# Kernel tuning notes

Measured on AMD Instinct MI355X. Metric: run time of the kernel, lower is better.

## Reference

```python
import jax, jax.numpy as jnp
import numpy as np
from jax import lax

B, L = 4, 1024
D_MODEL, D_INNER, D_STATE, D_CONV, DT_RANK, N_LAYERS = 256, 512, 16, 4, 16, 4
BN_EPS = 1e-5


def setup_inputs() -> dict:
    key = jax.random.key(0)
    ks = jax.random.split(key, 16)
    nrm = lambda k, s, sc: jax.random.normal(k, s, jnp.float32) * sc
    inp = {
        "x": nrm(ks[0], (B, L), 1.0),
        "y": nrm(ks[1], (B, L), 1.0),  # accepted but unused by forward
        # embedding: Conv1d(1 -> D_MODEL, k=3, same, no bias) + BatchNorm1d (inference stats) + SiLU
        "emb_w": nrm(ks[2], (D_MODEL, 1, 3), 1.0 / np.sqrt(3.0)),
        "bn_gamma": 1.0 + nrm(ks[3], (D_MODEL,), 0.1),
        "bn_beta": nrm(ks[4], (D_MODEL,), 0.1),
        "bn_mean": nrm(ks[5], (D_MODEL,), 0.1),
        "bn_var": jax.random.uniform(ks[6], (D_MODEL,), jnp.float32, 0.5, 1.5),
        # stacked Mamba layer params (leading dim = layer)
        "in_proj_w": nrm(ks[7], (N_LAYERS, 2 * D_INNER, D_MODEL), 1.0 / np.sqrt(D_MODEL)),
        "conv_w": nrm(ks[8], (N_LAYERS, D_INNER, 1, D_CONV), 1.0 / np.sqrt(D_CONV)),
        "conv_b": nrm(ks[9], (N_LAYERS, D_INNER), 0.02),
        "x_proj_w": nrm(ks[10], (N_LAYERS, DT_RANK + 2 * D_STATE, D_INNER), 1.0 / np.sqrt(D_INNER)),
        "dt_proj_w": nrm(ks[11], (N_LAYERS, D_INNER, DT_RANK), 1.0 / np.sqrt(DT_RANK)),
        # inverse-softplus of dt in [1e-3, 0.1] (mamba init)
        "dt_proj_b": jnp.log(jnp.expm1(jax.random.uniform(ks[12], (N_LAYERS, D_INNER), jnp.float32, 1e-3, 0.1))),
        # S4D-real init: A = -[1..N]
        "A_log": jnp.log(jnp.tile(jnp.arange(1, D_STATE + 1, dtype=jnp.float32)[None, None, :], (N_LAYERS, D_INNER, 1))),
        "D_skip": jnp.ones((N_LAYERS, D_INNER), jnp.float32),
        "out_proj_w": nrm(ks[13], (N_LAYERS, D_MODEL, D_INNER), 1.0 / np.sqrt(D_INNER)),
    }
    return inp


def selective_scan(u, dt, A, Bc, Cc, D_skip):
    # u, dt: (B,L,Di); A: (Di,N); Bc, Cc: (B,L,N)
    dA = jnp.exp(dt[..., None] * A)                              # (B,L,Di,N)
    dBu = dt[..., None] * Bc[:, :, None, :] * u[..., None]       # (B,L,Di,N)

    def step(h, xs):
        dA_t, dBu_t, C_t = xs
        h = dA_t * h + dBu_t                                      # (B,Di,N)
        y_t = jnp.einsum('bdn,bn->bd', h, C_t)
        return h, y_t

    h0 = jnp.zeros((u.shape[0], u.shape[2], A.shape[1]), u.dtype)
    _, ys = lax.scan(step, h0, (dA.swapaxes(0, 1), dBu.swapaxes(0, 1), Cc.swapaxes(0, 1)))
    return ys.swapaxes(0, 1) + u * D_skip                         # (B,L,Di)


def mamba_block(h, in_w, cw, cb, xp_w, dtp_w, dtp_b, A_log, D_skip, out_w):
    xz = jnp.einsum('bld,ed->ble', h, in_w)                       # (B,L,2Di)
    xi, z = jnp.split(xz, 2, axis=-1)
    # causal depthwise conv1d over time
    xc = lax.conv_general_dilated(xi.swapaxes(1, 2), cw, (1,), [(D_CONV - 1, 0)],
                                  dimension_numbers=('NCH', 'OIH', 'NCH'),
                                  feature_group_count=D_INNER) + cb[None, :, None]
    xc = jax.nn.silu(xc).swapaxes(1, 2)                           # (B,L,Di)
    xdbl = jnp.einsum('bld,ed->ble', xc, xp_w)                    # (B,L,dt_rank+2N)
    dt, Bc, Cc = jnp.split(xdbl, [DT_RANK, DT_RANK + D_STATE], axis=-1)
    dt = jax.nn.softplus(jnp.einsum('blr,dr->bld', dt, dtp_w) + dtp_b)
    A = -jnp.exp(A_log)                                           # (Di,N)
    y = selective_scan(xc, dt, A, Bc, Cc, D_skip)
    y = y * jax.nn.silu(z)
    return jnp.einsum('bld,od->blo', y, out_w)                    # (B,L,D_MODEL)


def reference(x, y, emb_w, bn_gamma, bn_beta, bn_mean, bn_var, in_proj_w, conv_w,
              conv_b, x_proj_w, dt_proj_w, dt_proj_b, A_log, D_skip, out_proj_w):
    h = x[:, None, :]                                             # (B,1,L)
    h = lax.conv_general_dilated(h, emb_w, (1,), 'SAME', dimension_numbers=('NCH', 'OIH', 'NCH'))
    inv = lax.rsqrt(bn_var + BN_EPS)
    h = (h - bn_mean[None, :, None]) * (inv * bn_gamma)[None, :, None] + bn_beta[None, :, None]
    h = jax.nn.silu(h).swapaxes(1, 2)                             # (B,L,D_MODEL)
    for i in range(N_LAYERS):
        h = mamba_block(h, in_proj_w[i], conv_w[i], conv_b[i], x_proj_w[i],
                        dt_proj_w[i], dt_proj_b[i], A_log[i], D_skip[i], out_proj_w[i])
    return h.sum(axis=-1)                                         # (B,L)
```

## Files before the change

kernel.cpp:

```cpp
#include <hip/hip_runtime.h>
#include <math.h>

#define BATCH 4
#define SEQL 1024
#define DMODEL 256
#define DINNER 512
#define DSTATE 16
#define DTRANK 16
#define NLAYERS 4
#define MTOT (BATCH * SEQL)

#define IDX(t) ((((t) & 63) * 17) + ((t) >> 6))

#define LOG2E 1.44269504088896340736f

typedef float v2f __attribute__((ext_vector_type(2)));

static __device__ __forceinline__ v2f pkfma(v2f a, v2f b, v2f c) {
    return __builtin_elementwise_fma(a, b, c);
}
static __device__ __forceinline__ float exp2fast(float x) {
    return __builtin_amdgcn_exp2f(x);
}
static __device__ __forceinline__ float siluf(float x) {
    return x / (1.0f + __expf(-x));
}
static __device__ __forceinline__ float softplusf(float x) {
    return (x > 0.0f) ? (x + __logf(1.0f + __expf(-x))) : __logf(1.0f + __expf(x));
}

__global__ void k_embed(const float* __restrict__ x, const float* __restrict__ emb_w,
                        const float* __restrict__ gamma, const float* __restrict__ beta,
                        const float* __restrict__ mean, const float* __restrict__ var,
                        float* __restrict__ h) {
    const int m = blockIdx.x;
    const int d = threadIdx.x;
    const int b = m >> 10;
    const int l = m & 1023;
    const float xm1 = (l > 0)    ? x[b * SEQL + l - 1] : 0.0f;
    const float x0  =              x[b * SEQL + l];
    const float xp1 = (l < 1023) ? x[b * SEQL + l + 1] : 0.0f;
    float c = xm1 * emb_w[d * 3 + 0] + x0 * emb_w[d * 3 + 1] + xp1 * emb_w[d * 3 + 2];
    const float inv = 1.0f / sqrtf(var[d] + 1e-5f);
    c = (c - mean[d]) * (inv * gamma[d]) + beta[d];
    h[(size_t)m * DMODEL + d] = siluf(c);
}

template <int BM, int BN, int BK, int TM, int TN, bool AKM, int KTOT, int KSPLIT>
__global__ __launch_bounds__((BM / TM) * (BN / TN))
void sgemm2(const float* __restrict__ A, int lda,
            const float* __restrict__ Bw, int ldb,
            float* __restrict__ C, int ldc, int mstride) {
    constexpr int TX = BN / TN;
    constexpr int TY = BM / TM;
    constexpr int NT = TX * TY;
    static_assert(NT == 256, "expect 256 threads");
    constexpr int KS = KTOT / KSPLIT;
    static_assert(KS % BK == 0, "");
    constexpr int NSTEPS = KS / BK;
    constexpr int A4 = BM * BK / 4;
    constexpr int B4 = BN * BK / 4;
    constexpr int APT = (A4 + NT - 1) / NT;
    constexpr int BPT = (B4 + NT - 1) / NT;
    constexpr bool AG = (A4 % NT) != 0;
    constexpr bool BG = (B4 % NT) != 0;

    const int tid = threadIdx.x;
    const int tx = tid % TX;
    const int ty = tid / TX;
    const int m0 = blockIdx.y * BM;
    const int n0 = blockIdx.x * BN;
    const int kt0 = blockIdx.z * KS;

    __shared__ float As[BK][BM + 4];
    __shared__ float Bs[BK][BN + 4];

    float acc[TM][TN] = {};
    float4 ra[APT], rb[BPT];

    auto loadA = [&](int kt) {
#pragma unroll
        for (int u = 0; u < APT; ++u) {
            const int v = tid + u * NT;
            if (!AG || v < A4) {
                if (AKM) {
                    const int kk = v / (BM / 4);
                    const int i4 = v % (BM / 4);
                    ra[u] = *reinterpret_cast<const float4*>(
                        &A[(size_t)(kt + kk) * lda + m0 + i4 * 4]);
                } else {
                    const int i = v / (BK / 4);
                    const int jv = v % (BK / 4);
                    ra[u] = *reinterpret_cast<const float4*>(
                        &A[(size_t)(m0 + i) * lda + kt + jv * 4]);
                }
            }
        }
    };
    auto loadB = [&](int kt) {
#pragma unroll
        for (int u = 0; u < BPT; ++u) {
            const int v = tid + u * NT;
            if (!BG || v < B4) {
                const int i = v / (BK / 4);
                const int jv = v % (BK / 4);
                rb[u] = *reinterpret_cast<const float4*>(
                    &Bw[(size_t)(n0 + i) * ldb + kt + jv * 4]);
            }
        }
    };
    auto storeAB = [&]() {
#pragma unroll
        for (int u = 0; u < APT; ++u) {
            const int v = tid + u * NT;
            if (!AG || v < A4) {
                if (AKM) {
                    const int kk = v / (BM / 4);
                    const int i4 = v % (BM / 4);
                    *reinterpret_cast<float4*>(&As[kk][i4 * 4]) = ra[u];
                } else {
                    const int i = v / (BK / 4);
                    const int jv = v % (BK / 4);
                    As[jv * 4 + 0][i] = ra[u].x;
                    As[jv * 4 + 1][i] = ra[u].y;
                    As[jv * 4 + 2][i] = ra[u].z;
                    As[jv * 4 + 3][i] = ra[u].w;
                }
            }
        }
#pragma unroll
        for (int u = 0; u < BPT; ++u) {
            const int v = tid + u * NT;
            if (!BG || v < B4) {
                const int i = v / (BK / 4);
                const int jv = v % (BK / 4);
                Bs[jv * 4 + 0][i] = rb[u].x;
                Bs[jv * 4 + 1][i] = rb[u].y;
                Bs[jv * 4 + 2][i] = rb[u].z;
                Bs[jv * 4 + 3][i] = rb[u].w;
            }
        }
    };

    loadA(kt0);
    loadB(kt0);

    for (int s = 0; s < NSTEPS; ++s) {
        storeAB();
        __syncthreads();
        if (s + 1 < NSTEPS) {
            loadA(kt0 + (s + 1) * BK);
            loadB(kt0 + (s + 1) * BK);
        }
#pragma unroll
        for (int k = 0; k < BK; ++k) {
            float a[TM], b[TN];
#pragma unroll
            for (int i = 0; i < TM; ++i) a[i] = As[k][ty * TM + i];
#pragma unroll
            for (int j = 0; j < TN; ++j) b[j] = Bs[k][tx * TN + j];
#pragma unroll
            for (int i = 0; i < TM; ++i)
#pragma unroll
                for (int j = 0; j < TN; ++j) acc[i][j] = fmaf(a[i], b[j], acc[i][j]);
        }
        __syncthreads();
    }

    float* Cz = C + (size_t)blockIdx.z * mstride;
#pragma unroll
    for (int i = 0; i < TM; ++i) {
        const int m = m0 + ty * TM + i;
#pragma unroll
        for (int j = 0; j < TN; ++j) {
            const int n = n0 + tx * TN + j;
            Cz[(size_t)m * ldc + n] = acc[i][j];
        }
    }
}

template <int BM, int BN, int BK, int TM, int TN, bool AKM, int KTOT, int KSPLIT>
__global__ __launch_bounds__((BM / TM) * (BN / TN))
void sgemm3(const float* __restrict__ A, int lda,
            const float* __restrict__ Bw, int ldb,
            float* __restrict__ C, int ldc, int mstride) {
    constexpr int TX = BN / TN;
    constexpr int TY = BM / TM;
    constexpr int NT = TX * TY;
    static_assert(NT == 256, "expect 256 threads");
    static_assert(TN % 2 == 0, "packed needs even TN");
    constexpr int TN2 = TN / 2;
    constexpr int KS = KTOT / KSPLIT;
    static_assert(KS % BK == 0, "");
    constexpr int NSTEPS = KS / BK;
    constexpr int A4 = BM * BK / 4;
    constexpr int B4 = BN * BK / 4;
    constexpr int APT = (A4 + NT - 1) / NT;
    constexpr int BPT = (B4 + NT - 1) / NT;
    constexpr bool AG = (A4 % NT) != 0;
    constexpr bool BG = (B4 % NT) != 0;

    const int tid = threadIdx.x;
    const int tx = tid % TX;
    const int ty = tid / TX;
    const int m0 = blockIdx.y * BM;
    const int n0 = blockIdx.x * BN;
    const int kt0 = blockIdx.z * KS;

    __shared__ float As[BK][BM + 4];
    __shared__ float Bs[BK][BN + 4];

    v2f acc[TM][TN2] = {};
    float4 ra[APT], rb[BPT];

    auto loadA = [&](int kt) {
#pragma unroll
        for (int u = 0; u < APT; ++u) {
            const int v = tid + u * NT;
            if (!AG || v < A4) {
                if (AKM) {
                    const int kk = v / (BM / 4);
                    const int i4 = v % (BM / 4);
                    ra[u] = *reinterpret_cast<const float4*>(
                        &A[(size_t)(kt + kk) * lda + m0 + i4 * 4]);
                } else {
                    const int i = v / (BK / 4);
                    const int jv = v % (BK / 4);
                    ra[u] = *reinterpret_cast<const float4*>(
                        &A[(size_t)(m0 + i) * lda + kt + jv * 4]);
                }
            }
        }
    };
    auto loadB = [&](int kt) {
#pragma unroll
        for (int u = 0; u < BPT; ++u) {
            const int v = tid + u * NT;
            if (!BG || v < B4) {
                const int i = v / (BK / 4);
                const int jv = v % (BK / 4);
                rb[u] = *reinterpret_cast<const float4*>(
                    &Bw[(size_t)(n0 + i) * ldb + kt + jv * 4]);
            }
        }
    };
    auto storeAB = [&]() {
#pragma unroll
        for (int u = 0; u < APT; ++u) {
            const int v = tid + u * NT;
            if (!AG || v < A4) {
                if (AKM) {
                    const int kk = v / (BM / 4);
                    const int i4 = v % (BM / 4);
                    *reinterpret_cast<float4*>(&As[kk][i4 * 4]) = ra[u];
                } else {
                    const int i = v / (BK / 4);
                    const int jv = v % (BK / 4);
                    As[jv * 4 + 0][i] = ra[u].x;
                    As[jv * 4 + 1][i] = ra[u].y;
                    As[jv * 4 + 2][i] = ra[u].z;
                    As[jv * 4 + 3][i] = ra[u].w;
                }
            }
        }
#pragma unroll
        for (int u = 0; u < BPT; ++u) {
            const int v = tid + u * NT;
            if (!BG || v < B4) {
                const int i = v / (BK / 4);
                const int jv = v % (BK / 4);
                Bs[jv * 4 + 0][i] = rb[u].x;
                Bs[jv * 4 + 1][i] = rb[u].y;
                Bs[jv * 4 + 2][i] = rb[u].z;
                Bs[jv * 4 + 3][i] = rb[u].w;
            }
        }
    };

    loadA(kt0);
    loadB(kt0);

    for (int s = 0; s < NSTEPS; ++s) {
        storeAB();
        __syncthreads();
        if (s + 1 < NSTEPS) {
            loadA(kt0 + (s + 1) * BK);
            loadB(kt0 + (s + 1) * BK);
        }
#pragma unroll
        for (int k = 0; k < BK; ++k) {
            float a[TM];
            v2f b2[TN2];
#pragma unroll
            for (int i = 0; i < TM; ++i) a[i] = As[k][ty * TM + i];
#pragma unroll
            for (int j = 0; j < TN2; ++j)
                b2[j] = *reinterpret_cast<const v2f*>(&Bs[k][tx * TN + 2 * j]);
#pragma unroll
            for (int i = 0; i < TM; ++i) {
                v2f av;
                av.x = a[i]; av.y = a[i];
#pragma unroll
                for (int j = 0; j < TN2; ++j) acc[i][j] = pkfma(av, b2[j], acc[i][j]);
            }
        }
        __syncthreads();
    }

    float* Cz = C + (size_t)blockIdx.z * mstride;
#pragma unroll
    for (int i = 0; i < TM; ++i) {
        const int m = m0 + ty * TM + i;
#pragma unroll
        for (int j = 0; j < TN2; ++j) {
            *reinterpret_cast<v2f*>(&Cz[(size_t)m * ldc + n0 + tx * TN + 2 * j]) =
                acc[i][j];
        }
    }
}

template <int KS>
__global__ __launch_bounds__(512) void k_kred(const float* __restrict__ part,
                                              float* __restrict__ out, int n4) {
    const int i = blockIdx.x * 512 + threadIdx.x;
    if (i >= n4) return;
    const float4* p = reinterpret_cast<const float4*>(part);
    float4 s = p[i];
#pragma unroll
    for (int z = 1; z < KS; ++z) {
        const float4 t = p[i + (size_t)z * n4];
        s.x += t.x; s.y += t.y; s.z += t.z; s.w += t.w;
    }
    reinterpret_cast<float4*>(out)[i] = s;
}

__global__ __launch_bounds__(256) void k_convT4(const float* __restrict__ xzT,
                                                const float* __restrict__ cw,
                                                const float* __restrict__ cb,
                                                float* __restrict__ xcT) {
    const int d = blockIdx.x;
    const int b = blockIdx.y;
    const float w0 = cw[d * 4 + 0], w1 = cw[d * 4 + 1];
    const float w2 = cw[d * 4 + 2], w3 = cw[d * 4 + 3];
    const float bias = cb[d];
    const float* row = xzT + (size_t)d * MTOT + b * SEQL;
    float* orow = xcT + (size_t)d * MTOT + b * SEQL;
    const int t4 = threadIdx.x * 4;
    const float4 xv = *reinterpret_cast<const float4*>(&row[t4]);
    float4 xm = make_float4(0.f, 0.f, 0.f, 0.f);
    if (t4 >= 4) xm = *reinterpret_cast<const float4*>(&row[t4 - 4]);
    float4 o;
    o.x = fmaf(xv.x, w3, fmaf(xm.w, w2, fmaf(xm.z, w1, fmaf(xm.y, w0, bias))));
    o.y = fmaf(xv.y, w3, fmaf(xv.x, w2, fmaf(xm.w, w1, fmaf(xm.z, w0, bias))));
    o.z = fmaf(xv.z, w3, fmaf(xv.y, w2, fmaf(xv.x, w1, fmaf(xm.w, w0, bias))));
    o.w = fmaf(xv.w, w3, fmaf(xv.z, w2, fmaf(xv.y, w1, fmaf(xv.x, w0, bias))));
    o.x = siluf(o.x); o.y = siluf(o.y); o.z = siluf(o.z); o.w = siluf(o.w);
    *reinterpret_cast<float4*>(&orow[t4]) = o;
}

#define CCH 64
#define CT 16

__global__ __launch_bounds__(256) void k_scan10(
    const float* __restrict__ xcT, const float* __restrict__ xdbl,
    const float* __restrict__ xzT, const float* __restrict__ dtw,
    const float* __restrict__ dtb, const float* __restrict__ A_log,
    const float* __restrict__ D_skip, float* __restrict__ yT) {
    const int d = blockIdx.x;
    const int b = blockIdx.y;
    const int tid = threadIdx.x;
    const int c = tid >> 2;
    const int nq = tid & 3;

    __shared__ float dt_s[1088];
    __shared__ float u_s[1088];
    __shared__ __align__(16) float PSp[CCH][20];
    __shared__ __align__(16) float PSs[CCH][20];

    const int mbase = b * SEQL;

    const float4 w0 = *reinterpret_cast<const float4*>(&dtw[d * 16 + 0]);
    const float4 w1 = *reinterpret_cast<const float4*>(&dtw[d * 16 + 4]);
    const float4 w2 = *reinterpret_cast<const float4*>(&dtw[d * 16 + 8]);
    const float4 w3 = *reinterpret_cast<const float4*>(&dtw[d * 16 + 12]);
    const float bias = dtb[d];

#pragma unroll
    for (int ph = 0; ph < 4; ++ph) {
        const int t = ph * 256 + tid;
        const float* xr = &xdbl[(size_t)(mbase + t) * 48];
        const float4 a0 = *reinterpret_cast<const float4*>(&xr[0]);
        const float4 a1 = *reinterpret_cast<const float4*>(&xr[4]);
        const float4 a2v = *reinterpret_cast<const float4*>(&xr[8]);
        const float4 a3 = *reinterpret_cast<const float4*>(&xr[12]);
        v2f s2; s2.x = bias; s2.y = 0.0f;
        v2f p, q;
        p.x = a0.x;  p.y = a0.y;  q.x = w0.x;  q.y = w0.y;  s2 = pkfma(p, q, s2);
        p.x = a0.z;  p.y = a0.w;  q.x = w0.z;  q.y = w0.w;  s2 = pkfma(p, q, s2);
        p.x = a1.x;  p.y = a1.y;  q.x = w1.x;  q.y = w1.y;  s2 = pkfma(p, q, s2);
        p.x = a1.z;  p.y = a1.w;  q.x = w1.z;  q.y = w1.w;  s2 = pkfma(p, q, s2);
        p.x = a2v.x; p.y = a2v.y; q.x = w2.x;  q.y = w2.y;  s2 = pkfma(p, q, s2);
        p.x = a2v.z; p.y = a2v.w; q.x = w2.z;  q.y = w2.w;  s2 = pkfma(p, q, s2);
        p.x = a3.x;  p.y = a3.y;  q.x = w3.x;  q.y = w3.y;  s2 = pkfma(p, q, s2);
        p.x = a3.z;  p.y = a3.w;  q.x = w3.z;  q.y = w3.w;  s2 = pkfma(p, q, s2);
        const float dt = softplusf(s2.x + s2.y);
        const float uv = xcT[(size_t)d * MTOT + mbase + t];
        dt_s[IDX(t)] = dt;
        u_s[IDX(t)]  = dt * uv;
    }
    __syncthreads();

    const float4 al = *reinterpret_cast<const float4*>(&A_log[d * DSTATE + nq * 4]);
    v2f a01, a23;
    a01.x = -__expf(al.x) * LOG2E;
    a01.y = -__expf(al.y) * LOG2E;
    a23.x = -__expf(al.z) * LOG2E;
    a23.y = -__expf(al.w) * LOG2E;

    const int t0 = c * CT;
    const int loc_base = (c & 3) * 272 + (c >> 2);

    const float* Bp = &xdbl[(size_t)(mbase + t0) * 48 + DTRANK + nq * 4];
    const float* Cp = Bp + DSTATE;

    float dtsum = 0.0f;
    v2f S01, S23;
    S01.x = S01.y = S23.x = S23.y = 0.0f;
#pragma unroll
    for (int j = 0; j < CT; ++j) {
        const float4 B4 = *reinterpret_cast<const float4*>(&Bp[j * 48]);
        const int loc = j * 17 + loc_base;
        const float dtv = dt_s[loc];
        const float du = u_s[loc];
        dtsum += dtv;
        v2f dd; dd.x = dtv; dd.y = dtv;
        v2f duv; duv.x = du; duv.y = du;
        const v2f t01 = dd * a01;
        const v2f t23 = dd * a23;
        v2f e01, e23;
        e01.x = exp2fast(t01.x); e01.y = exp2fast(t01.y);
        e23.x = exp2fast(t23.x); e23.y = exp2fast(t23.y);
        v2f B01, B23;
        B01.x = B4.x; B01.y = B4.y; B23.x = B4.z; B23.y = B4.w;
        S01 = pkfma(e01, S01, B01 * duv);
        S23 = pkfma(e23, S23, B23 * duv);
    }
    {
        float4 Pq, Sq;
        Pq.x = exp2fast(a01.x * dtsum);
        Pq.y = exp2fast(a01.y * dtsum);
        Pq.z = exp2fast(a23.x * dtsum);
        Pq.w = exp2fast(a23.y * dtsum);
        Sq.x = S01.x; Sq.y = S01.y; Sq.z = S23.x; Sq.w = S23.y;
        *reinterpret_cast<float4*>(&PSp[c][nq * 4]) = Pq;
        *reinterpret_cast<float4*>(&PSs[c][nq * 4]) = Sq;
    }
    __syncthreads();

    v2f h01, h23;
    h01.x = h01.y = h23.x = h23.y = 0.0f;
    for (int j = 0; j < c; ++j) {
        const float4 qp = *reinterpret_cast<const float4*>(&PSp[j][nq * 4]);
        const float4 qs = *reinterpret_cast<const float4*>(&PSs[j][nq * 4]);
        v2f pp, ss;
        pp.x = qp.x; pp.y = qp.y; ss.x = qs.x; ss.y = qs.y;
        h01 = pkfma(pp, h01, ss);
        pp.x = qp.z; pp.y = qp.w; ss.x = qs.z; ss.y = qs.w;
        h23 = pkfma(pp, h23, ss);
    }

#pragma unroll
    for (int j = 0; j < CT; ++j) {
        const float4 B4 = *reinterpret_cast<const float4*>(&Bp[j * 48]);
        const float4 C4 = *reinterpret_cast<const float4*>(&Cp[j * 48]);
        const int loc = j * 17 + loc_base;
        const float dtv = dt_s[loc];
        const float du = u_s[loc];
        v2f dd; dd.x = dtv; dd.y = dtv;
        v2f duv; duv.x = du; duv.y = du;
        const v2f t01 = dd * a01;
        const v2f t23 = dd * a23;
        v2f e01, e23;
        e01.x = exp2fast(t01.x); e01.y = exp2fast(t01.y);
        e23.x = exp2fast(t23.x); e23.y = exp2fast(t23.y);
        v2f B01, B23;
        B01.x = B4.x; B01.y = B4.y; B23.x = B4.z; B23.y = B4.w;
        h01 = pkfma(e01, h01, B01 * duv);
        h23 = pkfma(e23, h23, B23 * duv);
        v2f C01, C23;
        C01.x = C4.x; C01.y = C4.y; C23.x = C4.z; C23.y = C4.w;
        v2f tt = h01 * C01;
        tt = pkfma(h23, C23, tt);
        float p = tt.x + tt.y;
        p += __shfl_xor(p, 1);
        p += __shfl_xor(p, 2);
        if (nq == 0) dt_s[loc] = p;
    }
    __syncthreads();

    const float Dsk = D_skip[d];
#pragma unroll
    for (int ph = 0; ph < 4; ++ph) {
        const int t = ph * 256 + tid;
        const float uv = xcT[(size_t)d * MTOT + mbase + t];
        const float zv = xzT[(size_t)(DINNER + d) * MTOT + mbase + t];
        yT[(size_t)d * MTOT + mbase + t] = (dt_s[IDX(t)] + uv * Dsk) * siluf(zv);
    }
}

__global__ void k_wsum(const float* __restrict__ w, float* __restrict__ wsum) {
    const int d = threadIdx.x;
    float s = 0.0f;
    for (int o = 0; o < DMODEL; ++o) s += w[(size_t)o * DINNER + d];
    wsum[d] = s;
}

__global__ __launch_bounds__(256) void k_finalT(const float* __restrict__ yT,
                                                const float* __restrict__ wsum,
                                                float* __restrict__ out) {
    const int tid = threadIdx.x;
    const int dg = tid >> 5;
    const int ml = tid & 31;
    const int m = blockIdx.x * 32 + ml;
    float acc = 0.0f;
    const int dbase = dg * 64;
#pragma unroll 8
    for (int dd = 0; dd < 64; ++dd)
        acc = fmaf(yT[(size_t)(dbase + dd) * MTOT + m], wsum[dbase + dd], acc);
    __shared__ float red[8][33];
    red[dg][ml] = acc;
    __syncthreads();
    if (dg == 0) {
        float s = 0.0f;
#pragma unroll
        for (int g = 0; g < 8; ++g) s += red[g][ml];
        out[m] = s;
    }
}

extern "C" void kernel_launch(void* const* d_in, const int* in_sizes, int n_in,
                              void* d_out, int out_size, void* d_ws, size_t ws_size,
                              hipStream_t stream) {
    const float* x        = (const float*)d_in[0];
    const float* emb_w    = (const float*)d_in[2];
    const float* bn_gamma = (const float*)d_in[3];
    const float* bn_beta  = (const float*)d_in[4];
    const float* bn_mean  = (const float*)d_in[5];
    const float* bn_var   = (const float*)d_in[6];
    const float* in_proj_w  = (const float*)d_in[7];
    const float* conv_w     = (const float*)d_in[8];
    const float* conv_b     = (const float*)d_in[9];
    const float* x_proj_w   = (const float*)d_in[10];
    const float* dt_proj_w  = (const float*)d_in[11];
    const float* dt_proj_b  = (const float*)d_in[12];
    const float* A_log      = (const float*)d_in[13];
    const float* D_skip     = (const float*)d_in[14];
    const float* out_proj_w = (const float*)d_in[15];
    float* out = (float*)d_out;
    float* ws = (float*)d_ws;

    float* h    = ws;
    float* xzT  = h + (size_t)MTOT * DMODEL;
    float* xcT  = xzT + (size_t)1024 * MTOT;
    float* xdbl = xcT + (size_t)DINNER * MTOT;
    float* yT   = xdbl + (size_t)MTOT * 48;
    float* wsum = yT + (size_t)DINNER * MTOT;
    float* partX = yT;
    float* partO = xzT;

    k_embed<<<MTOT, DMODEL, 0, stream>>>(x, emb_w, bn_gamma, bn_beta, bn_mean, bn_var, h);

    for (int i = 0; i < NLAYERS; ++i) {
        const float* in_w  = in_proj_w + (size_t)i * 2 * DINNER * DMODEL;
        const float* cw    = conv_w + (size_t)i * DINNER * 4;
        const float* cb    = conv_b + (size_t)i * DINNER;
        const float* xp_w  = x_proj_w + (size_t)i * 48 * DINNER;
        const float* dtp_w = dt_proj_w + (size_t)i * DINNER * DTRANK;
        const float* dtp_b = dt_proj_b + (size_t)i * DINNER;
        const float* Al    = A_log + (size_t)i * DINNER * DSTATE;
        const float* Dsk   = D_skip + (size_t)i * DINNER;
        const float* o_w   = out_proj_w + (size_t)i * DMODEL * DINNER;

        sgemm3<64, 128, 16, 4, 8, false, DMODEL, 1>
            <<<dim3(MTOT / 128, 1024 / 64, 1), 256, 0, stream>>>(
                in_w, DMODEL, h, DMODEL, xzT, MTOT, 0);

        k_convT4<<<dim3(DINNER, BATCH), 256, 0, stream>>>(xzT, cw, cb, xcT);

        sgemm2<64, 48, 16, 4, 3, true, DINNER, 8>
            <<<dim3(1, MTOT / 64, 8), 256, 0, stream>>>(
                xcT, MTOT, xp_w, DINNER, partX, 48, MTOT * 48);
        k_kred<8><<<(MTOT * 48 / 4 + 511) / 512, 512, 0, stream>>>(
            partX, xdbl, MTOT * 48 / 4);

        k_scan10<<<dim3(DINNER, BATCH), 256, 0, stream>>>(
            xcT, xdbl, xzT, dtp_w, dtp_b, Al, Dsk, yT);

        if (i < NLAYERS - 1) {
            sgemm3<64, 64, 16, 4, 4, true, DINNER, 2>
                <<<dim3(DMODEL / 64, MTOT / 64, 2), 256, 0, stream>>>(
                    yT, MTOT, o_w, DINNER, partO, DMODEL, MTOT * DMODEL);
            k_kred<2><<<(MTOT * DMODEL / 4 + 511) / 512, 512, 0, stream>>>(
                partO, h, MTOT * DMODEL / 4);
        } else {
            k_wsum<<<1, DINNER, 0, stream>>>(o_w, wsum);
            k_finalT<<<MTOT / 32, 256, 0, stream>>>(yT, wsum, out);
        }
    }
}
```

Before: 438.0 us.

## Fuse causal conv into x_proj and scan, fold split-K reduce into in_proj

Removes the standalone depthwise conv kernel and the xcT buffer: the conv+SiLU is recomputed inline when loading the A tile of the x_proj GEMM and again in the scan kernel from xzT. The out_proj split-K partial reduction kernel is dropped by summing the two partial buffers while loading the B operand of the next layer's in_proj GEMM, with partO given its own workspace region. This saves several launches and a full read/write pass of intermediate activations, at the cost of redundant conv arithmetic and extra scalar loads in the scan.

```diff
diff --git a/kernel.cpp b/kernel.cpp
--- a/kernel.cpp
+++ b/kernel.cpp
@@ -46,15 +46,18 @@
     h[(size_t)m * DMODEL + d] = siluf(c);
 }
 
-template <int BM, int BN, int BK, int TM, int TN, bool AKM, int KTOT, int KSPLIT>
+template <int BM, int BN, int BK, int TM, int TN, bool AKM, int KTOT, int KSPLIT,
+          bool BSUM>
 __global__ __launch_bounds__((BM / TM) * (BN / TN))
-void sgemm2(const float* __restrict__ A, int lda,
-            const float* __restrict__ Bw, int ldb,
+void sgemm3(const float* __restrict__ A, int lda,
+            const float* __restrict__ Bw, const float* __restrict__ Bw2, int ldb,
             float* __restrict__ C, int ldc, int mstride) {
     constexpr int TX = BN / TN;
     constexpr int TY = BM / TM;
     constexpr int NT = TX * TY;
     static_assert(NT == 256, "expect 256 threads");
+    static_assert(TN % 2 == 0, "packed needs even TN");
+    constexpr int TN2 = TN / 2;
     constexpr int KS = KTOT / KSPLIT;
     static_assert(KS % BK == 0, "");
     constexpr int NSTEPS = KS / BK;
@@ -75,7 +78,7 @@
     __shared__ float As[BK][BM + 4];
     __shared__ float Bs[BK][BN + 4];
 
-    float acc[TM][TN] = {};
+    v2f acc[TM][TN2] = {};
     float4 ra[APT], rb[BPT];
 
     auto loadA = [&](int kt) {
@@ -104,8 +107,13 @@
             if (!BG || v < B4) {
                 const int i = v / (BK / 4);
                 const int jv = v % (BK / 4);
-                rb[u] = *reinterpret_cast<const float4*>(
-                    &Bw[(size_t)(n0 + i) * ldb + kt + jv * 4]);
+                const size_t off = (size_t)(n0 + i) * ldb + kt + jv * 4;
+                rb[u] = *reinterpret_cast<const float4*>(&Bw[off]);
+                if (BSUM) {
+                    const float4 t2 = *reinterpret_cast<const float4*>(&Bw2[off]);
+                    rb[u].x += t2.x; rb[u].y += t2.y;
+                    rb[u].z += t2.z; rb[u].w += t2.w;
+                }
             }
         }
     };
@@ -154,15 +162,20 @@
         }
 #pragma unroll
         for (int k = 0; k < BK; ++k) {
-            float a[TM], b[TN];
+            float a[TM];
+            v2f b2[TN2];
 #pragma unroll
             for (int i = 0; i < TM; ++i) a[i] = As[k][ty * TM + i];
 #pragma unroll
-            for (int j = 0; j < TN; ++j) b[j] = Bs[k][tx * TN + j];
-#pragma unroll
-            for (int i = 0; i < TM; ++i)
-#pragma unroll
-                for (int j = 0; j < TN; ++j) acc[i][j] = fmaf(a[i], b[j], acc[i][j]);
+            for (int j = 0; j < TN2; ++j)
+                b2[j] = *reinterpret_cast<const v2f*>(&Bs[k][tx * TN + 2 * j]);
+#pragma unroll
+            for (int i = 0; i < TM; ++i) {
+                v2f av;
+                av.x = a[i]; av.y = a[i];
+#pragma unroll
+                for (int j = 0; j < TN2; ++j) acc[i][j] = pkfma(av, b2[j], acc[i][j]);
+            }
         }
         __syncthreads();
     }
@@ -172,108 +185,74 @@
     for (int i = 0; i < TM; ++i) {
         const int m = m0 + ty * TM + i;
 #pragma unroll
-        for (int j = 0; j < TN; ++j) {
-            const int n = n0 + tx * TN + j;
-            Cz[(size_t)m * ldc + n] = acc[i][j];
-        }
-    }
-}
-
-template <int BM, int BN, int BK, int TM, int TN, bool AKM, int KTOT, int KSPLIT>
-__global__ __launch_bounds__((BM / TM) * (BN / TN))
-void sgemm3(const float* __restrict__ A, int lda,
-            const float* __restrict__ Bw, int ldb,
-            float* __restrict__ C, int ldc, int mstride) {
+        for (int j = 0; j < TN2; ++j) {
+            *reinterpret_cast<v2f*>(&Cz[(size_t)m * ldc + n0 + tx * TN + 2 * j]) =
+                acc[i][j];
+        }
+    }
+}
+
+__global__ __launch_bounds__(256)
+void sgemm_xp(const float* __restrict__ xzT, const float* __restrict__ cw,
+              const float* __restrict__ cb, const float* __restrict__ Bw,
+              float* __restrict__ C, int mstride) {
+    constexpr int BM = 64, BN = 48, BK = 16, TM = 4, TN = 3;
     constexpr int TX = BN / TN;
-    constexpr int TY = BM / TM;
-    constexpr int NT = TX * TY;
-    static_assert(NT == 256, "expect 256 threads");
-    static_assert(TN % 2 == 0, "packed needs even TN");
-    constexpr int TN2 = TN / 2;
-    constexpr int KS = KTOT / KSPLIT;
-    static_assert(KS % BK == 0, "");
+    constexpr int KS = DINNER / 8;
     constexpr int NSTEPS = KS / BK;
-    constexpr int A4 = BM * BK / 4;
     constexpr int B4 = BN * BK / 4;
-    constexpr int APT = (A4 + NT - 1) / NT;
-    constexpr int BPT = (B4 + NT - 1) / NT;
-    constexpr bool AG = (A4 % NT) != 0;
-    constexpr bool BG = (B4 % NT) != 0;
 
     const int tid = threadIdx.x;
     const int tx = tid % TX;
     const int ty = tid / TX;
     const int m0 = blockIdx.y * BM;
-    const int n0 = blockIdx.x * BN;
     const int kt0 = blockIdx.z * KS;
 
     __shared__ float As[BK][BM + 4];
     __shared__ float Bs[BK][BN + 4];
 
-    v2f acc[TM][TN2] = {};
-    float4 ra[APT], rb[BPT];
+    float acc[TM][TN] = {};
+    float4 ra;
+    float4 rb;
 
     auto loadA = [&](int kt) {
-#pragma unroll
-        for (int u = 0; u < APT; ++u) {
-            const int v = tid + u * NT;
-            if (!AG || v < A4) {
-                if (AKM) {
-                    const int kk = v / (BM / 4);
-                    const int i4 = v % (BM / 4);
-                    ra[u] = *reinterpret_cast<const float4*>(
-                        &A[(size_t)(kt + kk) * lda + m0 + i4 * 4]);
-                } else {
-                    const int i = v / (BK / 4);
-                    const int jv = v % (BK / 4);
-                    ra[u] = *reinterpret_cast<const float4*>(
-                        &A[(size_t)(m0 + i) * lda + kt + jv * 4]);
-                }
-            }
-        }
+        const int kk = tid >> 4;
+        const int i4 = tid & 15;
+        const int r = kt + kk;
+        const float* row = xzT + (size_t)r * MTOT;
+        const int t4 = m0 + i4 * 4;
+        const float4 xv = *reinterpret_cast<const float4*>(&row[t4]);
+        float4 xm = make_float4(0.f, 0.f, 0.f, 0.f);
+        if ((t4 & 1023) >= 4) xm = *reinterpret_cast<const float4*>(&row[t4 - 4]);
+        const float4 w = *reinterpret_cast<const float4*>(&cw[r * 4]);
+        const float bias = cb[r];
+        float4 o;
+        o.x = fmaf(xv.x, w.w, fmaf(xm.w, w.z, fmaf(xm.z, w.y, fmaf(xm.y, w.x, bias))));
+        o.y = fmaf(xv.y, w.w, fmaf(xv.x, w.z, fmaf(xm.w, w.y, fmaf(xm.z, w.x, bias))));
+        o.z = fmaf(xv.z, w.w, fmaf(xv.y, w.z, fmaf(xv.x, w.y, fmaf(xm.w, w.x, bias))));
+        o.w = fmaf(xv.w, w.w, fmaf(xv.z, w.z, fmaf(xv.y, w.y, fmaf(xv.x, w.x, bias))));
+        o.x = siluf(o.x); o.y = siluf(o.y); o.z = siluf(o.z); o.w = siluf(o.w);
+        ra = o;
     };
     auto loadB = [&](int kt) {
-#pragma unroll
-        for (int u = 0; u < BPT; ++u) {
-            const int v = tid + u * NT;
-            if (!BG || v < B4) {
-                const int i = v / (BK / 4);
-                const int jv = v % (BK / 4);
-                rb[u] = *reinterpret_cast<const float4*>(
-                    &Bw[(size_t)(n0 + i) * ldb + kt + jv * 4]);
-            }
+        if (tid < B4) {
+            const int i = tid / (BK / 4);
+            const int jv = tid % (BK / 4);
+            rb = *reinterpret_cast<const float4*>(
+                &Bw[(size_t)i * DINNER + kt + jv * 4]);
         }
     };
     auto storeAB = [&]() {
-#pragma unroll
-        for (int u = 0; u < APT; ++u) {
-            const int v = tid + u * NT;
-            if (!AG || v < A4) {
-                if (AKM) {
-                    const int kk = v / (BM / 4);
-                    const int i4 = v % (BM / 4);
-                    *reinterpret_cast<float4*>(&As[kk][i4 * 4]) = ra[u];
-                } else {
-                    const int i = v / (BK / 4);
-                    const int jv = v % (BK / 4);
-                    As[jv * 4 + 0][i] = ra[u].x;
-                    As[jv * 4 + 1][i] = ra[u].y;
-                    As[jv * 4 + 2][i] = ra[u].z;
-                    As[jv * 4 + 3][i] = ra[u].w;
-                }
-            }
-        }
-#pragma unroll
-        for (int u = 0; u < BPT; ++u) {
-            const int v = tid + u * NT;
-            if (!BG || v < B4) {
-                const int i = v / (BK / 4);
-                const int jv = v % (BK / 4);
-                Bs[jv * 4 + 0][i] = rb[u].x;
-                Bs[jv * 4 + 1][i] = rb[u].y;
-                Bs[jv * 4 + 2][i] = rb[u].z;
-                Bs[jv * 4 + 3][i] = rb[u].w;
-            }
+        const int kk = tid >> 4;
+        const int i4 = tid & 15;
+        *reinterpret_cast<float4*>(&As[kk][i4 * 4]) = ra;
+        if (tid < B4) {
+            const int i = tid / (BK / 4);
+            const int jv = tid % (BK / 4);
+            Bs[jv * 4 + 0][i] = rb.x;
+            Bs[jv * 4 + 1][i] = rb.y;
+            Bs[jv * 4 + 2][i] = rb.z;
+            Bs[jv * 4 + 3][i] = rb.w;
         }
     };
 
@@ -289,20 +268,15 @@
         }
 #pragma unroll
         for (int k = 0; k < BK; ++k) {
-            float a[TM];
-            v2f b2[TN2];
+            float a[TM], b[TN];
 #pragma unroll
             for (int i = 0; i < TM; ++i) a[i] = As[k][ty * TM + i];
 #pragma unroll
-            for (int j = 0; j < TN2; ++j)
-                b2[j] = *reinterpret_cast<const v2f*>(&Bs[k][tx * TN + 2 * j]);
-#pragma unroll
-            for (int i = 0; i < TM; ++i) {
-                v2f av;
-                av.x = a[i]; av.y = a[i];
-#pragma unroll
-                for (int j = 0; j < TN2; ++j) acc[i][j] = pkfma(av, b2[j], acc[i][j]);
-            }
+            for (int j = 0; j < TN; ++j) b[j] = Bs[k][tx * TN + j];
+#pragma unroll
+            for (int i = 0; i < TM; ++i)
+#pragma unroll
+                for (int j = 0; j < TN; ++j) acc[i][j] = fmaf(a[i], b[j], acc[i][j]);
         }
         __syncthreads();
     }
@@ -312,10 +286,8 @@
     for (int i = 0; i < TM; ++i) {
         const int m = m0 + ty * TM + i;
 #pragma unroll
-        for (int j = 0; j < TN2; ++j) {
-            *reinterpret_cast<v2f*>(&Cz[(size_t)m * ldc + n0 + tx * TN + 2 * j]) =
-                acc[i][j];
-        }
+        for (int j = 0; j < TN; ++j)
+            Cz[(size_t)m * 48 + tx * TN + j] = acc[i][j];
     }
 }
 
@@ -334,38 +306,15 @@
     reinterpret_cast<float4*>(out)[i] = s;
 }
 
-__global__ __launch_bounds__(256) void k_convT4(const float* __restrict__ xzT,
-                                                const float* __restrict__ cw,
-                                                const float* __restrict__ cb,
-                                                float* __restrict__ xcT) {
-    const int d = blockIdx.x;
-    const int b = blockIdx.y;
-    const float w0 = cw[d * 4 + 0], w1 = cw[d * 4 + 1];
-    const float w2 = cw[d * 4 + 2], w3 = cw[d * 4 + 3];
-    const float bias = cb[d];
-    const float* row = xzT + (size_t)d * MTOT + b * SEQL;
-    float* orow = xcT + (size_t)d * MTOT + b * SEQL;
-    const int t4 = threadIdx.x * 4;
-    const float4 xv = *reinterpret_cast<const float4*>(&row[t4]);
-    float4 xm = make_float4(0.f, 0.f, 0.f, 0.f);
-    if (t4 >= 4) xm = *reinterpret_cast<const float4*>(&row[t4 - 4]);
-    float4 o;
-    o.x = fmaf(xv.x, w3, fmaf(xm.w, w2, fmaf(xm.z, w1, fmaf(xm.y, w0, bias))));
-    o.y = fmaf(xv.y, w3, fmaf(xv.x, w2, fmaf(xm.w, w1, fmaf(xm.z, w0, bias))));
-    o.z = fmaf(xv.z, w3, fmaf(xv.y, w2, fmaf(xv.x, w1, fmaf(xm.w, w0, bias))));
-    o.w = fmaf(xv.w, w3, fmaf(xv.z, w2, fmaf(xv.y, w1, fmaf(xv.x, w0, bias))));
-    o.x = siluf(o.x); o.y = siluf(o.y); o.z = siluf(o.z); o.w = siluf(o.w);
-    *reinterpret_cast<float4*>(&orow[t4]) = o;
-}
-
 #define CCH 64
 #define CT 16
 
-__global__ __launch_bounds__(256) void k_scan10(
-    const float* __restrict__ xcT, const float* __restrict__ xdbl,
-    const float* __restrict__ xzT, const float* __restrict__ dtw,
-    const float* __restrict__ dtb, const float* __restrict__ A_log,
-    const float* __restrict__ D_skip, float* __restrict__ yT) {
+__global__ __launch_bounds__(256) void k_scan11(
+    const float* __restrict__ xdbl, const float* __restrict__ xzT,
+    const float* __restrict__ dtw, const float* __restrict__ dtb,
+    const float* __restrict__ cw, const float* __restrict__ cb,
+    const float* __restrict__ A_log, const float* __restrict__ D_skip,
+    float* __restrict__ yT) {
     const int d = blockIdx.x;
     const int b = blockIdx.y;
     const int tid = threadIdx.x;
@@ -378,12 +327,15 @@
     __shared__ __align__(16) float PSs[CCH][20];
 
     const int mbase = b * SEQL;
+    const float* xrow = xzT + (size_t)d * MTOT + mbase;
 
     const float4 w0 = *reinterpret_cast<const float4*>(&dtw[d * 16 + 0]);
     const float4 w1 = *reinterpret_cast<const float4*>(&dtw[d * 16 + 4]);
     const float4 w2 = *reinterpret_cast<const float4*>(&dtw[d * 16 + 8]);
     const float4 w3 = *reinterpret_cast<const float4*>(&dtw[d * 16 + 12]);
     const float bias = dtb[d];
+    const float4 cwv = *reinterpret_cast<const float4*>(&cw[d * 4]);
+    const float cbias = cb[d];
 
 #pragma unroll
     for (int ph = 0; ph < 4; ++ph) {
@@ -404,7 +356,13 @@
         p.x = a3.x;  p.y = a3.y;  q.x = w3.x;  q.y = w3.y;  s2 = pkfma(p, q, s2);
         p.x = a3.z;  p.y = a3.w;  q.x = w3.z;  q.y = w3.w;  s2 = pkfma(p, q, s2);
         const float dt = softplusf(s2.x + s2.y);
-        const float uv = xcT[(size_t)d * MTOT + mbase + t];
+        const float xt  = xrow[t];
+        const float xt1 = (t >= 1) ? xrow[t - 1] : 0.0f;
+        const float xt2 = (t >= 2) ? xrow[t - 2] : 0.0f;
+        const float xt3 = (t >= 3) ? xrow[t - 3] : 0.0f;
+        float cv = fmaf(xt, cwv.w, fmaf(xt1, cwv.z,
+                   fmaf(xt2, cwv.y, fmaf(xt3, cwv.x, cbias))));
+        const float uv = siluf(cv);
         dt_s[IDX(t)] = dt;
         u_s[IDX(t)]  = dt * uv;
     }
@@ -502,7 +460,13 @@
 #pragma unroll
     for (int ph = 0; ph < 4; ++ph) {
         const int t = ph * 256 + tid;
-        const float uv = xcT[(size_t)d * MTOT + mbase + t];
+        const float xt  = xrow[t];
+        const float xt1 = (t >= 1) ? xrow[t - 1] : 0.0f;
+        const float xt2 = (t >= 2) ? xrow[t - 2] : 0.0f;
+        const float xt3 = (t >= 3) ? xrow[t - 3] : 0.0f;
+        float cv = fmaf(xt, cwv.w, fmaf(xt1, cwv.z,
+                   fmaf(xt2, cwv.y, fmaf(xt3, cwv.x, cbias))));
+        const float uv = siluf(cv);
         const float zv = xzT[(size_t)(DINNER + d) * MTOT + mbase + t];
         yT[(size_t)d * MTOT + mbase + t] = (dt_s[IDX(t)] + uv * Dsk) * siluf(zv);
     }
@@ -559,14 +523,13 @@
     float* out = (float*)d_out;
     float* ws = (float*)d_ws;
 
-    float* h    = ws;
-    float* xzT  = h + (size_t)MTOT * DMODEL;
-    float* xcT  = xzT + (size_t)1024 * MTOT;
-    float* xdbl = xcT + (size_t)DINNER * MTOT;
-    float* yT   = xdbl + (size_t)MTOT * 48;
-    float* wsum = yT + (size_t)DINNER * MTOT;
+    float* h     = ws;
+    float* xzT   = h + (size_t)MTOT * DMODEL;
+    float* partO = xzT + (size_t)1024 * MTOT;
+    float* xdbl  = partO + (size_t)2 * MTOT * DMODEL;
+    float* yT    = xdbl + (size_t)MTOT * 48;
+    float* wsum  = yT + (size_t)DINNER * MTOT;
     float* partX = yT;
-    float* partO = xzT;
 
     k_embed<<<MTOT, DMODEL, 0, stream>>>(x, emb_w, bn_gamma, bn_beta, bn_mean, bn_var, h);
 
@@ -581,27 +544,29 @@
         const float* Dsk   = D_skip + (size_t)i * DINNER;
         const float* o_w   = out_proj_w + (size_t)i * DMODEL * DINNER;
 
-        sgemm3<64, 128, 16, 4, 8, false, DMODEL, 1>
-            <<<dim3(MTOT / 128, 1024 / 64, 1), 256, 0, stream>>>(
-                in_w, DMODEL, h, DMODEL, xzT, MTOT, 0);
-
-        k_convT4<<<dim3(DINNER, BATCH), 256, 0, stream>>>(xzT, cw, cb, xcT);
-
-        sgemm2<64, 48, 16, 4, 3, true, DINNER, 8>
-            <<<dim3(1, MTOT / 64, 8), 256, 0, stream>>>(
-                xcT, MTOT, xp_w, DINNER, partX, 48, MTOT * 48);
+        if (i == 0) {
+            sgemm3<64, 128, 16, 4, 8, false, DMODEL, 1, false>
+                <<<dim3(MTOT / 128, 1024 / 64, 1), 256, 0, stream>>>(
+                    in_w, DMODEL, h, h, DMODEL, xzT, MTOT, 0);
+        } else {
+            sgemm3<64, 128, 16, 4, 8, false, DMODEL, 1, true>
+                <<<dim3(MTOT / 128, 1024 / 64, 1), 256, 0, stream>>>(
+                    in_w, DMODEL, partO, partO + (size_t)MTOT * DMODEL, DMODEL,
+                    xzT, MTOT, 0);
+        }
+
+        sgemm_xp<<<dim3(1, MTOT / 64, 8), 256, 0, stream>>>(
+            xzT, cw, cb, xp_w, partX, MTOT * 48);
         k_kred<8><<<(MTOT * 48 / 4 + 511) / 512, 512, 0, stream>>>(
             partX, xdbl, MTOT * 48 / 4);
 
-        k_scan10<<<dim3(DINNER, BATCH), 256, 0, stream>>>(
-            xcT, xdbl, xzT, dtp_w, dtp_b, Al, Dsk, yT);
+        k_scan11<<<dim3(DINNER, BATCH), 256, 0, stream>>>(
+            xdbl, xzT, dtp_w, dtp_b, cw, cb, Al, Dsk, yT);
 
         if (i < NLAYERS - 1) {
-            sgemm3<64, 64, 16, 4, 4, true, DINNER, 2>
+            sgemm3<64, 64, 16, 4, 4, true, DINNER, 2, false>
                 <<<dim3(DMODEL / 64, MTOT / 64, 2), 256, 0, stream>>>(
-                    yT, MTOT, o_w, DINNER, partO, DMODEL, MTOT * DMODEL);
-            k_kred<2><<<(MTOT * DMODEL / 4 + 511) / 512, 512, 0, stream>>>(
-                partO, h, MTOT * DMODEL / 4);
+                    yT, MTOT, o_w, o_w, DINNER, partO, DMODEL, MTOT * DMODEL);
         } else {
             k_wsum<<<1, DINNER, 0, stream>>>(o_w, wsum);
             k_finalT<<<MTOT / 32, 256, 0, stream>>>(yT, wsum, out);
```

After: 423.2 us. -3.4%, faster.
